# Optimization experiments

Measured on AMD Instinct MI355X. Metric: run time of the kernel, lower is better.

Reference implementation:

```python
import jax, jax.numpy as jnp
import numpy as np
from jax import lax

B, L, H, E, V = 16, 128, 1024, 512, 32000
MAX_LENGTH = 128
SOS_INDEX = 1
NUM_LAYERS = 2


def setup_inputs() -> dict:
    key = jax.random.key(0)
    ks = jax.random.split(key, 16)
    inp = {}
    inp['input_tensor'] = jax.random.randint(ks[0], (B, L), 0, V)
    inp['target_tensor'] = jax.random.randint(ks[1], (B, L), 0, V)
    inp['true_sample'] = 1
    s = lambda k, shape, fan: jax.random.normal(k, shape, jnp.float32) / np.float32(np.sqrt(fan))
    inp['embedding'] = jax.random.normal(ks[2], (V, E), jnp.float32) * 0.02
    inp['enc_W'] = s(ks[3], (E, H), E)
    inp['enc_b'] = jnp.zeros((H,), jnp.float32)
    inp['Wih0'] = s(ks[4], (E, 3 * H), E)
    inp['Whh0'] = s(ks[5], (H, 3 * H), H)
    inp['bih0'] = jnp.zeros((3 * H,), jnp.float32)
    inp['bhh0'] = jnp.zeros((3 * H,), jnp.float32)
    inp['Wih1'] = s(ks[6], (H, 3 * H), H)
    inp['Whh1'] = s(ks[7], (H, 3 * H), H)
    inp['bih1'] = jnp.zeros((3 * H,), jnp.float32)
    inp['bhh1'] = jnp.zeros((3 * H,), jnp.float32)
    inp['W_out'] = s(ks[8], (2 * H, V), 2 * H)
    inp['b_out'] = jnp.zeros((V,), jnp.float32)
    return inp


def _gru_cell(x, h, Wih, Whh, bih, bhh):
    gx = x @ Wih + bih
    gh = h @ Whh + bhh
    xr, xz, xn = jnp.split(gx, 3, axis=-1)
    hr, hz, hn = jnp.split(gh, 3, axis=-1)
    r = jax.nn.sigmoid(xr + hr)
    z = jax.nn.sigmoid(xz + hz)
    n = jnp.tanh(xn + r * hn)
    return (1.0 - z) * n + z * h


def _forward(input_tensor, true_sample, embedding, enc_W, enc_b,
             Wih0, Whh0, bih0, bhh0, Wih1, Whh1, bih1, bhh1, W_out, b_out):
    batch_size, input_length = input_tensor.shape
    target_length = input_length
    # Encoder: embed + per-timestep projection -> [B, L, H]
    enc_emb = embedding[input_tensor]
    enc_hidden = jnp.tanh(enc_emb @ enc_W + enc_b)
    enc_hidden_t = jnp.transpose(enc_hidden, (1, 0, 2))  # [L, B, H]
    # Pad at the front to max_length (mirrors the copy loop)
    encoder_outputs = jnp.zeros((MAX_LENGTH, batch_size, H), enc_hidden.dtype)
    encoder_outputs = encoder_outputs.at[MAX_LENGTH - input_length:].set(enc_hidden_t)
    # Decoder initial hidden: last encoder state stacked over layers
    h_init = enc_hidden_t[-1]  # [B, H]
    # NOTE: original never updates decoder_input inside the loop -> constant SOS
    x0 = jnp.broadcast_to(embedding[SOS_INDEX], (batch_size, E))
    inv_sqrt_h = np.float32(1.0 / np.sqrt(H))

    def step(carry, _):
        h0, h1 = carry
        h0 = _gru_cell(x0, h0, Wih0, Whh0, bih0, bhh0)
        h1 = _gru_cell(h0, h1, Wih1, Whh1, bih1, bhh1)
        scores = jnp.einsum('bh,lbh->bl', h1, encoder_outputs) * inv_sqrt_h
        attn = jax.nn.softmax(scores, axis=-1)
        ctx = jnp.einsum('bl,lbh->bh', attn, encoder_outputs)
        logits = jnp.concatenate([h1, ctx], axis=-1) @ W_out + b_out
        return (h0, h1), jax.nn.sigmoid(logits)

    _, probs = lax.scan(step, (h_init, h_init), None, length=target_length)
    decoder_outputs = jnp.transpose(probs, (1, 0, 2))  # [B, T, V]
    # Scalar gather: p[b,w] = decoder_outputs[b, w, input_tensor[b, w]]
    out_probabilities = jnp.take_along_axis(decoder_outputs, input_tensor[..., None], axis=2)[..., 0]
    target = jnp.full(input_tensor.shape, np.float32(int(true_sample)), jnp.float32)
    p = jnp.clip(out_probabilities, 1e-12, 1.0 - 1e-7)
    bce = -(target * jnp.log(p) + (1.0 - target) * jnp.log1p(-p))
    loss = jnp.mean(bce) / np.float32(batch_size)
    return loss, out_probabilities


def reference(input_tensor, target_tensor, true_sample, embedding, enc_W, enc_b,
              Wih0, Whh0, bih0, bhh0, Wih1, Whh1, bih1, bhh1, W_out, b_out):
    return _forward(input_tensor, true_sample, embedding, enc_W, enc_b,
                    Wih0, Whh0, bih0, bhh0, Wih1, Whh1, bih1, bhh1, W_out, b_out)
```

## Files before the change

kernel.cpp:

```cpp
#include <hip/hip_runtime.h>
#include <math.h>

#define BB 16
#define LL 128
#define HH 1024
#define EE 512
#define VV 32000
#define G3 3072
#define NBLK 256

__device__ __forceinline__ float sigmoidf_(float x){ return 1.0f/(1.0f+expf(-x)); }

__device__ __forceinline__ float red64(float v){
  v += __shfl_xor(v, 1, 64); v += __shfl_xor(v, 2, 64);
  v += __shfl_xor(v, 4, 64); v += __shfl_xor(v, 8, 64);
  v += __shfl_xor(v, 16, 64); v += __shfl_xor(v, 32, 64);
  return v;
}
__device__ __forceinline__ float red32(float v){
  v += __shfl_xor(v, 1, 64); v += __shfl_xor(v, 2, 64);
  v += __shfl_xor(v, 4, 64); v += __shfl_xor(v, 8, 64);
  v += __shfl_xor(v, 16, 64);
  return v;
}

__global__ void k_rowidx(const int* __restrict__ inp, int* __restrict__ idx){
  int r = blockIdx.x*256 + threadIdx.x;
  if (r < 2048){ int l = r >> 4, b = r & 15; idx[r] = inp[b*LL + l]; }
}

template<int ACT, int KK>
__global__ __launch_bounds__(256) void k_gemm(const float* __restrict__ A, const int* __restrict__ rowidx,
                       const float* __restrict__ Bm, const float* __restrict__ bias,
                       float* __restrict__ C, int N){
  constexpr int KS = (KK==512)?9:10;
  __shared__ float As[32*KK];
  const int tid = threadIdx.x;
  const int r0 = blockIdx.x*32;
  const int c  = blockIdx.y*512 + (tid<<1);
  for (int i = tid; i < 32*KK; i += 256){
    int rr = i >> KS;
    int row = r0 + rr;
    int arow = rowidx ? rowidx[row] : row;
    int kk = i - (rr<<KS);
    As[i] = A[(size_t)arow*KK + kk];
  }
  __syncthreads();
  float2 acc[32];
  #pragma unroll
  for (int r=0;r<32;r++){ acc[r].x=0.f; acc[r].y=0.f; }
  for (int k=0;k<KK;k++){
    const float2 w = *(const float2*)(Bm + (size_t)k*N + c);
    #pragma unroll
    for (int r=0;r<32;r++){
      float a = As[(r<<KS)+k];
      acc[r].x = fmaf(a,w.x,acc[r].x);
      acc[r].y = fmaf(a,w.y,acc[r].y);
    }
  }
  const float2 bv = *(const float2*)(bias + c);
  #pragma unroll
  for (int r=0;r<32;r++){
    float x = acc[r].x + bv.x, y = acc[r].y + bv.y;
    if (ACT==1){ x = tanhf(x); y = tanhf(y); }
    *(float2*)(C + (size_t)(r0+r)*N + c) = make_float2(x,y);
  }
}

__global__ __launch_bounds__(512,1) void k_chains(
    const float* enclast, float* H0all, float* H1all,
    const float* __restrict__ Whh0, const float* __restrict__ Whh1,
    const float* __restrict__ Wih0, const float* __restrict__ Wih1,
    const float* __restrict__ emb,
    const float* __restrict__ bih0, const float* __restrict__ bhh0,
    const float* __restrict__ bhh1, const float* __restrict__ bih1,
    int* flagsB, int* flagsA)
{
  __shared__ float w0l[12][1024];
  __shared__ float w1l[12][1024];
  __shared__ float wil[12][1024];
  __shared__ float gxbuf[16*12];
  const int tid  = threadIdx.x;
  const int jb   = blockIdx.x << 2;
  const int waveid = tid >> 6;
  const int cgA = waveid >> 2;
  const int bgA = waveid & 3;
  const int kgA = tid & 63;
  const int koffA = kgA << 2;
  const int b0A = bgA << 2;
  const int cgB = waveid >> 1;
  const int bgB = ((waveid & 1) << 1) | ((tid >> 5) & 1);
  const int kgB = tid & 31;
  const int koffB = kgB << 2;
  const int b0B = bgB << 2;
  const int mB  = cgB >> 1;

  const bool pwA = (kgA < 8);
  const int  jlA = (cgA << 1) + (kgA & 1);
  const int  jpA = jb + jlA;
  const int  biA = (kgA >> 1) & 3;
  const int  bA  = b0A + biA;
  const bool pwB = (cgB >= 2) && (kgB < 8);
  const int  jlB = ((cgB & 1) << 1) + (kgB & 1);
  const int  jpB = jb + jlB;
  const int  biB = (kgB >> 1) & 3;
  const int  bB  = b0B + biB;

  float g0r=0.f, g0z=0.f, g0n=0.f;
  {
    for (int idx = tid; idx < 1536; idx += 512){
      int g = idx >> 9, k = idx & 511;
      float4 a = *(const float4*)(Wih0 + (size_t)k*G3 + g*1024 + jb);
      w0l[g*4+0][k]=a.x; w0l[g*4+1][k]=a.y; w0l[g*4+2][k]=a.z; w0l[g*4+3][k]=a.w;
    }
    __syncthreads();
    const float* e1 = emb + EE;
    float ag[6];
    #pragma unroll
    for (int cl=0;cl<6;cl++) ag[cl]=0.f;
    #pragma unroll
    for (int u=0;u<2;u++){
      float4 e = *(const float4*)(e1 + u*256 + koffA);
      #pragma unroll
      for (int cl=0;cl<6;cl++){
        const int gc = ((cl>>1)<<2) + (cgA<<1) + (cl&1);
        const float4 w = *(const float4*)(&w0l[gc][u*256 + koffA]);
        float v = ag[cl];
        v=fmaf(w.x,e.x,v); v=fmaf(w.y,e.y,v); v=fmaf(w.z,e.z,v); v=fmaf(w.w,e.w,v);
        ag[cl]=v;
      }
    }
    #pragma unroll
    for (int cl=0;cl<6;cl++) ag[cl] = red64(ag[cl]);
    if (pwA){
      const int jj = kgA & 1;
      g0r = (jj ? ag[1] : ag[0]) + bih0[jpA];
      g0z = (jj ? ag[3] : ag[2]) + bih0[1024+jpA];
      g0n = (jj ? ag[5] : ag[4]) + bih0[2048+jpA];
    }
    __syncthreads();
  }

  for (int idx = tid; idx < 3072; idx += 512){
    int g = idx >> 10, k = idx & 1023;
    float4 a = *(const float4*)(Whh0 + (size_t)k*G3 + g*1024 + jb);
    w0l[g*4+0][k]=a.x; w0l[g*4+1][k]=a.y; w0l[g*4+2][k]=a.z; w0l[g*4+3][k]=a.w;
    float4 d = *(const float4*)(Whh1 + (size_t)k*G3 + g*1024 + jb);
    w1l[g*4+0][k]=d.x; w1l[g*4+1][k]=d.y; w1l[g*4+2][k]=d.z; w1l[g*4+3][k]=d.w;
    float4 e = *(const float4*)(Wih1 + (size_t)k*G3 + g*1024 + jb);
    wil[g*4+0][k]=e.x; wil[g*4+1][k]=e.y; wil[g*4+2][k]=e.z; wil[g*4+3][k]=e.w;
  }
  float b0rA=0.f,b0zA=0.f,b0nA=0.f;
  if (pwA){ b0rA = bhh0[jpA]; b0zA = bhh0[1024+jpA]; b0nA = bhh0[2048+jpA]; }
  float birB=0.f,bizB=0.f,binB=0.f,b1rB=0.f,b1zB=0.f,b1nB=0.f;
  if (pwB){
    birB = bih1[jpB]; bizB = bih1[1024+jpB]; binB = bih1[2048+jpB];
    b1rB = bhh1[jpB]; b1zB = bhh1[1024+jpB]; b1nB = bhh1[2048+jpB];
  }
  __syncthreads();

  const int myflag = (int)blockIdx.x * 32;
  const int pollfl = (tid & 255) * 32;

  for (int t = 0; t <= LL+1; ++t){
    if (t >= 1){
      while (__hip_atomic_load(&flagsB[pollfl], __ATOMIC_RELAXED,
                               __HIP_MEMORY_SCOPE_AGENT) < t)
        __builtin_amdgcn_s_sleep(1);
      __syncthreads();
    }

    if (t >= 2){
      const float* hp0 = H0all + (size_t)(t-2)*(BB*HH);
      const float* hp1 = (t==2) ? enclast : (H1all + (size_t)(t-3)*(BB*HH));
      const float* hr  = mB ? hp1 : hp0;
      float hprev1 = 0.f;
      if (pwB) hprev1 = hp1[(size_t)bB*HH + jpB];

      float accB[6][4];
      #pragma unroll
      for (int cl=0;cl<6;cl++)
        #pragma unroll
        for (int bi=0;bi<4;bi++) accB[cl][bi]=0.f;

      #pragma unroll
      for (int u=0;u<8;u++){
        float4 h4[4];
        #pragma unroll
        for (int bi=0;bi<4;bi++)
          h4[bi] = *(const float4*)(hr + (size_t)(b0B+bi)*HH + u*128 + koffB);
        #pragma unroll
        for (int cl=0;cl<6;cl++){
          const int gc = ((cl>>1)<<2) + ((cgB&1)<<1) + (cl&1);
          const float4 w = mB ? *(const float4*)(&w1l[gc][u*128 + koffB])
                              : *(const float4*)(&wil[gc][u*128 + koffB]);
          #pragma unroll
          for (int bi=0;bi<4;bi++){
            float v = accB[cl][bi];
            v=fmaf(w.x,h4[bi].x,v); v=fmaf(w.y,h4[bi].y,v);
            v=fmaf(w.z,h4[bi].z,v); v=fmaf(w.w,h4[bi].w,v);
            accB[cl][bi]=v;
          }
        }
      }
      #pragma unroll
      for (int cl=0;cl<6;cl++)
        #pragma unroll
        for (int bi=0;bi<4;bi++) accB[cl][bi] = red32(accB[cl][bi]);

      if (mB == 0){
        #pragma unroll
        for (int cl=0;cl<6;cl++){
          if (kgB == cl){
            const int g = cl >> 1;
            const int jl = ((cgB&1)<<1) + (cl&1);
            #pragma unroll
            for (int bi=0;bi<4;bi++)
              gxbuf[(b0B+bi)*12 + g*4 + jl] = accB[cl][bi];
          }
        }
      }
      __syncthreads();
      if (pwB){
        float ghr=0.f, ghz=0.f, ghn=0.f;
        #pragma unroll
        for (int jj=0;jj<2;jj++)
          #pragma unroll
          for (int ii=0;ii<4;ii++){
            bool sel = ((kgB&1)==jj) & (biB==ii);
            ghr = sel ? accB[jj][ii]   : ghr;
            ghz = sel ? accB[2+jj][ii] : ghz;
            ghn = sel ? accB[4+jj][ii] : ghn;
          }
        float gxr = gxbuf[bB*12 + 0*4 + jlB];
        float gxz = gxbuf[bB*12 + 1*4 + jlB];
        float gxn = gxbuf[bB*12 + 2*4 + jlB];
        float r = sigmoidf_(gxr + birB + ghr + b1rB);
        float z = sigmoidf_(gxz + bizB + ghz + b1zB);
        float n = tanhf    (gxn + binB + r*(ghn + b1nB));
        float hnew = (1.f-z)*n + z*hprev1;
        __hip_atomic_store((int*)&H1all[(size_t)(t-2)*(BB*HH) + (size_t)bB*HH + jpB],
                           __float_as_int(hnew),
                           __ATOMIC_RELAXED, __HIP_MEMORY_SCOPE_AGENT);
      }
    }

    asm volatile("s_waitcnt vmcnt(0)" ::: "memory");
    __syncthreads();
    if (tid == 0)
      __hip_atomic_store(&flagsB[myflag], t+1,
                         __ATOMIC_RELAXED, __HIP_MEMORY_SCOPE_AGENT);

    if (t >= 1){
      while (__hip_atomic_load(&flagsA[pollfl], __ATOMIC_RELAXED,
                               __HIP_MEMORY_SCOPE_AGENT) < t)
        __builtin_amdgcn_s_sleep(1);
      __syncthreads();
    }

    if (t < LL){
      const float* hp0 = (t==0) ? enclast : (H0all + (size_t)(t-1)*(BB*HH));
      float hprev0 = 0.f;
      if (pwA) hprev0 = hp0[(size_t)bA*HH + jpA];

      float acc0[6][4];
      #pragma unroll
      for (int cl=0;cl<6;cl++)
        #pragma unroll
        for (int bi=0;bi<4;bi++) acc0[cl][bi]=0.f;

      #pragma unroll
      for (int u=0;u<4;u++){
        float4 h4[4];
        #pragma unroll
        for (int bi=0;bi<4;bi++)
          h4[bi] = *(const float4*)(hp0 + (size_t)(b0A+bi)*HH + u*256 + koffA);
        #pragma unroll
        for (int cl=0;cl<6;cl++){
          const int gc = ((cl>>1)<<2) + (cgA<<1) + (cl&1);
          const float4 w = *(const float4*)(&w0l[gc][u*256 + koffA]);
          #pragma unroll
          for (int bi=0;bi<4;bi++){
            float v = acc0[cl][bi];
            v=fmaf(w.x,h4[bi].x,v); v=fmaf(w.y,h4[bi].y,v);
            v=fmaf(w.z,h4[bi].z,v); v=fmaf(w.w,h4[bi].w,v);
            acc0[cl][bi]=v;
          }
        }
      }
      #pragma unroll
      for (int cl=0;cl<6;cl++)
        #pragma unroll
        for (int bi=0;bi<4;bi++) acc0[cl][bi] = red64(acc0[cl][bi]);

      if (pwA){
        float ghr=0.f, ghz=0.f, ghn=0.f;
        #pragma unroll
        for (int jj=0;jj<2;jj++)
          #pragma unroll
          for (int ii=0;ii<4;ii++){
            bool sel = ((kgA&1)==jj) & (biA==ii);
            ghr = sel ? acc0[jj][ii]   : ghr;
            ghz = sel ? acc0[2+jj][ii] : ghz;
            ghn = sel ? acc0[4+jj][ii] : ghn;
          }
        float r = sigmoidf_(g0r + ghr + b0rA);
        float z = sigmoidf_(g0z + ghz + b0zA);
        float n = tanhf    (g0n + r*(ghn + b0nA));
        float hnew = (1.f-z)*n + z*hprev0;
        __hip_atomic_store((int*)&H0all[(size_t)t*(BB*HH) + (size_t)bA*HH + jpA],
                           __float_as_int(hnew),
                           __ATOMIC_RELAXED, __HIP_MEMORY_SCOPE_AGENT);
      }
    }

    asm volatile("s_waitcnt vmcnt(0)" ::: "memory");
    __syncthreads();
    if (tid == 0)
      __hip_atomic_store(&flagsA[myflag], t+1,
                         __ATOMIC_RELAXED, __HIP_MEMORY_SCOPE_AGENT);
  }
}

__global__ __launch_bounds__(256) void k_attn(const float* __restrict__ enc, const float* __restrict__ H1,
                       float* __restrict__ ctx){
  __shared__ float h1s[8][HH];
  __shared__ float sc[8][LL];
  __shared__ float part[2][8][LL];
  const int tid = threadIdx.x;
  const int s0 = blockIdx.x*8, b = blockIdx.y;
  for (int i = tid; i < 8*HH; i += 256){
    int si = i >> 10, k = i & 1023;
    h1s[si][k] = H1[(size_t)(s0+si)*BB*HH + (size_t)b*HH + k];
  }
  __syncthreads();
  {
    const int l = tid & 127, half = tid >> 7;
    const float4* er = (const float4*)(enc + ((size_t)l*BB + b)*HH + half*512);
    float a[8];
    #pragma unroll
    for (int s=0;s<8;s++) a[s]=0.f;
    for (int q=0;q<128;q++){
      float4 e = er[q];
      #pragma unroll
      for (int s=0;s<8;s++){
        const float4 h = *(const float4*)(&h1s[s][half*512 + q*4]);
        a[s] += h.x*e.x + h.y*e.y + h.z*e.z + h.w*e.w;
      }
    }
    #pragma unroll
    for (int s=0;s<8;s++) part[half][s][l] = a[s];
  }
  __syncthreads();
  for (int p = tid; p < 1024; p += 256){
    int s = p >> 7, l = p & 127;
    sc[s][l] = (part[0][s][l] + part[1][s][l]) * 0.03125f;
  }
  __syncthreads();
  {
    int s = tid >> 5, lid = tid & 31;
    float v0 = sc[s][lid], v1 = sc[s][lid+32], v2 = sc[s][lid+64], v3 = sc[s][lid+96];
    float m = fmaxf(fmaxf(v0,v1),fmaxf(v2,v3));
    for (int off=16; off>=1; off>>=1) m = fmaxf(m, __shfl_xor(m, off, 32));
    float e0=__expf(v0-m), e1=__expf(v1-m), e2=__expf(v2-m), e3=__expf(v3-m);
    float ssum = e0+e1+e2+e3;
    for (int off=16; off>=1; off>>=1) ssum += __shfl_xor(ssum, off, 32);
    float inv = 1.0f/ssum;
    sc[s][lid]=e0*inv; sc[s][lid+32]=e1*inv; sc[s][lid+64]=e2*inv; sc[s][lid+96]=e3*inv;
  }
  __syncthreads();
  {
    float acc[4][8];
    #pragma unroll
    for (int q=0;q<4;q++)
      #pragma unroll
      for (int s=0;s<8;s++) acc[q][s]=0.f;
    for (int l=0;l<128;l++){
      const float* er = enc + ((size_t)l*BB + b)*HH + tid;
      float a[8];
      #pragma unroll
      for (int s=0;s<8;s++) a[s] = sc[s][l];
      #pragma unroll
      for (int q=0;q<4;q++){
        float e = er[q*256];
        #pragma unroll
        for (int s=0;s<8;s++) acc[q][s] = fmaf(a[s], e, acc[q][s]);
      }
    }
    #pragma unroll
    for (int s=0;s<8;s++)
      #pragma unroll
      for (int q=0;q<4;q++)
        ctx[(size_t)(s0+s)*BB*HH + (size_t)b*HH + tid + q*256] = acc[q][s];
  }
}

__global__ __launch_bounds__(256) void k_logit(const float* __restrict__ H1, const float* __restrict__ ctx,
                        const float* __restrict__ Wout, const float* __restrict__ bout,
                        const int* __restrict__ inp, const int* __restrict__ ts,
                        float* __restrict__ outp, float* __restrict__ bce){
  __shared__ float rbuf[256];
  const int i = blockIdx.x;
  const int b = i >> 7, t = i & 127;
  const int v = inp[b*LL + t];
  const int tid = threadIdx.x;
  const float* h1r = H1 + ((size_t)t*BB + b)*HH;
  const float* cxr = ctx + ((size_t)t*BB + b)*HH;
  float acc = 0.f;
  #pragma unroll
  for (int q=0;q<4;q++){
    int k = tid + q*256;
    acc = fmaf(h1r[k], Wout[(size_t)k*VV + v], acc);
  }
  #pragma unroll
  for (int q=0;q<4;q++){
    int k = tid + q*256;
    acc = fmaf(cxr[k], Wout[(size_t)(k+1024)*VV + v], acc);
  }
  rbuf[tid] = acc;
  __syncthreads();
  for (int s=128; s>0; s>>=1){
    if (tid < s) rbuf[tid] += rbuf[tid+s];
    __syncthreads();
  }
  if (tid==0){
    float logit = rbuf[0] + bout[v];
    float p = 1.0f/(1.0f + expf(-logit));
    outp[b*LL + t] = p;
    float pc = fminf(fmaxf(p, 1e-12f), 1.0f - 1e-7f);
    float tg = (float)ts[0];
    bce[i] = -(tg*logf(pc) + (1.0f-tg)*log1pf(-pc));
  }
}

__global__ void k_loss(const float* __restrict__ bce, float* __restrict__ out0){
  __shared__ float rbuf[256];
  int tid = threadIdx.x;
  float s = 0.f;
  for (int i = tid; i < 2048; i += 256) s += bce[i];
  rbuf[tid] = s; __syncthreads();
  for (int st=128; st>0; st>>=1){
    if (tid<st) rbuf[tid]+=rbuf[tid+st];
    __syncthreads();
  }
  if (tid==0) out0[0] = rbuf[0] * (1.0f/(2048.0f*16.0f));
}

extern "C" void kernel_launch(void* const* d_in, const int* in_sizes, int n_in,
                              void* d_out, int out_size, void* d_ws, size_t ws_size,
                              hipStream_t stream){
  (void)in_sizes; (void)n_in; (void)out_size; (void)ws_size;
  const int*   inp   = (const int*)d_in[0];
  const int*   ts    = (const int*)d_in[2];
  const float* emb   = (const float*)d_in[3];
  const float* encW  = (const float*)d_in[4];
  const float* encb  = (const float*)d_in[5];
  const float* Wih0  = (const float*)d_in[6];
  const float* Whh0  = (const float*)d_in[7];
  const float* bih0  = (const float*)d_in[8];
  const float* bhh0  = (const float*)d_in[9];
  const float* Wih1  = (const float*)d_in[10];
  const float* Whh1  = (const float*)d_in[11];
  const float* bih1  = (const float*)d_in[12];
  const float* bhh1  = (const float*)d_in[13];
  const float* Wout  = (const float*)d_in[14];
  const float* bout  = (const float*)d_in[15];
  float* out = (float*)d_out;

  float* ws      = (float*)d_ws;
  float* enc_out = ws;
  float* H0      = enc_out + 2097152;
  float* H1      = H0 + 2097152;
  float* GX1     = H1 + 2097152;
  float* CTX     = GX1 + 6291456;
  float* gx0     = CTX + 2097152;
  float* bceb    = gx0 + 3072;
  int*   rowidx  = (int*)(bceb + 2048);
  int*   flagsB  = rowidx + 2048;
  int*   flagsA  = flagsB + 256*32;

  hipMemsetAsync(flagsB, 0, 512*32*sizeof(int), stream);
  k_rowidx<<<8,256,0,stream>>>(inp, rowidx);
  k_gemm<1,512><<<dim3(64,2),256,0,stream>>>(emb, rowidx, encW, encb, enc_out, HH);

  const float* enclast = enc_out + (size_t)127*BB*HH;

  k_chains<<<NBLK,512,0,stream>>>(enclast, H0, H1, Whh0, Whh1, Wih0, Wih1, emb,
                                  bih0, bhh0, bhh1, bih1, flagsB, flagsA);
  k_attn<<<dim3(16,16),256,0,stream>>>(enc_out, H1, CTX);
  k_logit<<<2048,256,0,stream>>>(H1, CTX, Wout, bout, inp, ts, out+1, bceb);
  k_loss<<<1,256,0,stream>>>(bceb, out);
}
```

Baseline: 2.089 ms.

## Merge GRU layer phases into one grid barrier per step via centralized go flag

The persistent GRU kernel now runs layer 1 for step t-1 and layer 0 for step t in the same phase, since both depend only on data from the previous phase. This leaves one grid-wide barrier per timestep instead of two and drops one loop iteration. The barrier itself changes from every block polling all 256 flags to block 0 gathering the flags and publishing a single go counter that the other blocks poll. The aim is to cut inter-block synchronization latency, at the cost of a two-hop barrier and more serial work per phase inside each block.

```diff
diff --git a/kernel.cpp b/kernel.cpp
--- a/kernel.cpp
+++ b/kernel.cpp
@@ -74,7 +74,7 @@
     const float* __restrict__ emb,
     const float* __restrict__ bih0, const float* __restrict__ bhh0,
     const float* __restrict__ bhh1, const float* __restrict__ bih1,
-    int* flagsB, int* flagsA)
+    int* flags, int* go)
 {
   __shared__ float w0l[12][1024];
   __shared__ float w1l[12][1024];
@@ -160,19 +160,31 @@
   __syncthreads();
 
   const int myflag = (int)blockIdx.x * 32;
-  const int pollfl = (tid & 255) * 32;
-
-  for (int t = 0; t <= LL+1; ++t){
+
+  for (int t = 0; t <= LL; ++t){
     if (t >= 1){
-      while (__hip_atomic_load(&flagsB[pollfl], __ATOMIC_RELAXED,
-                               __HIP_MEMORY_SCOPE_AGENT) < t)
-        __builtin_amdgcn_s_sleep(1);
-      __syncthreads();
-    }
-
-    if (t >= 2){
-      const float* hp0 = H0all + (size_t)(t-2)*(BB*HH);
-      const float* hp1 = (t==2) ? enclast : (H1all + (size_t)(t-3)*(BB*HH));
+      if (blockIdx.x == 0){
+        if (tid < 256){
+          while (__hip_atomic_load(&flags[tid*32], __ATOMIC_RELAXED,
+                                   __HIP_MEMORY_SCOPE_AGENT) < t)
+            __builtin_amdgcn_s_sleep(1);
+        }
+        __syncthreads();
+        if (tid == 0)
+          __hip_atomic_store(go, t, __ATOMIC_RELAXED, __HIP_MEMORY_SCOPE_AGENT);
+      } else {
+        if (tid == 0){
+          while (__hip_atomic_load(go, __ATOMIC_RELAXED,
+                                   __HIP_MEMORY_SCOPE_AGENT) < t)
+            __builtin_amdgcn_s_sleep(1);
+        }
+        __syncthreads();
+      }
+    }
+
+    if (t >= 1){
+      const float* hp0 = H0all + (size_t)(t-1)*(BB*HH);
+      const float* hp1 = (t==1) ? enclast : (H1all + (size_t)(t-2)*(BB*HH));
       const float* hr  = mB ? hp1 : hp0;
       float hprev1 = 0.f;
       if (pwB) hprev1 = hp1[(size_t)bB*HH + jpB];
@@ -239,23 +251,10 @@
         float z = sigmoidf_(gxz + bizB + ghz + b1zB);
         float n = tanhf    (gxn + binB + r*(ghn + b1nB));
         float hnew = (1.f-z)*n + z*hprev1;
-        __hip_atomic_store((int*)&H1all[(size_t)(t-2)*(BB*HH) + (size_t)bB*HH + jpB],
+        __hip_atomic_store((int*)&H1all[(size_t)(t-1)*(BB*HH) + (size_t)bB*HH + jpB],
                            __float_as_int(hnew),
                            __ATOMIC_RELAXED, __HIP_MEMORY_SCOPE_AGENT);
       }
-    }
-
-    asm volatile("s_waitcnt vmcnt(0)" ::: "memory");
-    __syncthreads();
-    if (tid == 0)
-      __hip_atomic_store(&flagsB[myflag], t+1,
-                         __ATOMIC_RELAXED, __HIP_MEMORY_SCOPE_AGENT);
-
-    if (t >= 1){
-      while (__hip_atomic_load(&flagsA[pollfl], __ATOMIC_RELAXED,
-                               __HIP_MEMORY_SCOPE_AGENT) < t)
-        __builtin_amdgcn_s_sleep(1);
-      __syncthreads();
     }
 
     if (t < LL){
@@ -314,11 +313,13 @@
       }
     }
 
-    asm volatile("s_waitcnt vmcnt(0)" ::: "memory");
-    __syncthreads();
-    if (tid == 0)
-      __hip_atomic_store(&flagsA[myflag], t+1,
-                         __ATOMIC_RELAXED, __HIP_MEMORY_SCOPE_AGENT);
+    if (t < LL){
+      asm volatile("s_waitcnt vmcnt(0)" ::: "memory");
+      __syncthreads();
+      if (tid == 0)
+        __hip_atomic_store(&flags[myflag], t+1,
+                           __ATOMIC_RELAXED, __HIP_MEMORY_SCOPE_AGENT);
+    }
   }
 }
 
@@ -476,17 +477,17 @@
   float* gx0     = CTX + 2097152;
   float* bceb    = gx0 + 3072;
   int*   rowidx  = (int*)(bceb + 2048);
-  int*   flagsB  = rowidx + 2048;
-  int*   flagsA  = flagsB + 256*32;
-
-  hipMemsetAsync(flagsB, 0, 512*32*sizeof(int), stream);
+  int*   flags   = rowidx + 2048;
+  int*   go      = flags + 256*32;
+
+  hipMemsetAsync(flags, 0, (256*32 + 32)*sizeof(int), stream);
   k_rowidx<<<8,256,0,stream>>>(inp, rowidx);
   k_gemm<1,512><<<dim3(64,2),256,0,stream>>>(emb, rowidx, encW, encb, enc_out, HH);
 
   const float* enclast = enc_out + (size_t)127*BB*HH;
 
   k_chains<<<NBLK,512,0,stream>>>(enclast, H0, H1, Whh0, Whh1, Wih0, Wih1, emb,
-                                  bih0, bhh0, bhh1, bih1, flagsB, flagsA);
+                                  bih0, bhh0, bhh1, bih1, flags, go);
   k_attn<<<dim3(16,16),256,0,stream>>>(enc_out, H1, CTX);
   k_logit<<<2048,256,0,stream>>>(H1, CTX, Wout, bout, inp, ts, out+1, bceb);
   k_loss<<<1,256,0,stream>>>(bceb, out);
```

New measurement: 2.070 ms. Within noise of the previous version (-0.9%).
